# Performance work log

Hardware: AMD Instinct MI355X
Metric: run time of the kernel (lower is better)

Reference implementation:

```python
import jax, jax.numpy as jnp
import numpy as np

N_NODES = 100000
N_EDGES = 3200000

def setup_inputs() -> dict:
    key = jax.random.key(0)
    ks = jax.random.split(key, 16)
    x = jax.random.normal(ks[0], (N_NODES, 3), dtype=jnp.float32)
    edge_index = jax.random.randint(ks[1], (2, N_EDGES), 0, N_NODES, dtype=jnp.int32)
    def glorot(k, shape):
        fan = shape[0] + shape[-1]
        lim = jnp.sqrt(6.0 / fan)
        return jax.random.uniform(k, shape, jnp.float32, -lim, lim)
    params = {
        'W1': glorot(ks[2], (3, 32)),  'as1': glorot(ks[3], (2, 16)), 'ad1': glorot(ks[4], (2, 16)), 'b1': jnp.zeros((32,), jnp.float32),
        'W2': glorot(ks[5], (32, 32)), 'as2': glorot(ks[6], (2, 16)), 'ad2': glorot(ks[7], (2, 16)), 'b2': jnp.zeros((32,), jnp.float32),
        'W3': glorot(ks[8], (32, 8)),  'as3': glorot(ks[9], (1, 8)),  'ad3': glorot(ks[10], (1, 8)), 'b3': jnp.zeros((8,), jnp.float32),
        'Wo': glorot(ks[11], (8, 1)),  'bo': jnp.zeros((1,), jnp.float32),
    }
    return dict(x=x, edge_index=edge_index, **params)

def _gat_layer(x, src, dst, W, a_src, a_dst, bias, n_heads, c_out):
    # PyG GATConv: linear -> per-head attention logits -> leaky_relu -> segment softmax over dst -> scatter-weighted sum -> concat heads + bias
    N = x.shape[0]
    h = (x @ W).reshape(N, n_heads, c_out)              # [N,H,C]
    al_s = jnp.sum(h * a_src[None], axis=-1)            # [N,H]
    al_d = jnp.sum(h * a_dst[None], axis=-1)            # [N,H]
    logits = jax.nn.leaky_relu(al_s[src] + al_d[dst], 0.2)  # [E,H]
    m = jax.ops.segment_max(logits, dst, num_segments=N)
    e = jnp.exp(logits - m[dst])
    s = jax.ops.segment_sum(e, dst, num_segments=N)
    alpha = e / (s[dst] + 1e-16)                        # [E,H]
    msg = h[src] * alpha[:, :, None]                    # [E,H,C]
    out = jax.ops.segment_sum(msg, dst, num_segments=N) # [N,H,C]
    return out.reshape(N, n_heads * c_out) + bias

def reference(x, edge_index, W1, as1, ad1, b1, W2, as2, ad2, b2, W3, as3, ad3, b3, Wo, bo):
    N = x.shape[0]
    # add self loops (PyG GATConv default add_self_loops=True)
    loop = jnp.arange(N, dtype=edge_index.dtype)
    src = jnp.concatenate([edge_index[0], loop])
    dst = jnp.concatenate([edge_index[1], loop])
    h = jax.nn.elu(_gat_layer(x, src, dst, W1, as1, ad1, b1, 2, 16))
    h = jax.nn.elu(_gat_layer(h, src, dst, W2, as2, ad2, b2, 2, 16))
    h = jax.nn.elu(_gat_layer(h, src, dst, W3, as3, ad3, b3, 1, 8))
    return h @ Wo + bo
```

## Files before the change

kernel.cpp:

```cpp
#include <hip/hip_runtime.h>
#include <hip/hip_bf16.h>
#include <math.h>

#define DEVINL __device__ __forceinline__

DEVINL float loadIn(const void* p, long i, int bf) {
    return bf ? __bfloat162float(((const __hip_bfloat16*)p)[i])
              : ((const float*)p)[i];
}

DEVINL float leaky(float v) { return fmaxf(v, 0.2f * v); }

DEVINL unsigned pack_bf16(float a, float b) {
    __hip_bfloat16 x = __float2bfloat16(a), y = __float2bfloat16(b);
    unsigned short ux = *reinterpret_cast<unsigned short*>(&x);
    unsigned short uy = *reinterpret_cast<unsigned short*>(&y);
    return (unsigned)ux | ((unsigned)uy << 16);
}
DEVINL float lo16(unsigned u) { return __uint_as_float(u << 16); }
DEVINL float hi16(unsigned u) { return __uint_as_float(u & 0xFFFF0000u); }

__global__ __launch_bounds__(1024) void prep(const unsigned* __restrict__ x,
                                             int* __restrict__ flag,
                                             int* __restrict__ bcnt) {
    __shared__ int sh[1024];
    int t = threadIdx.x;
    bcnt[t] = 0;
    int cnt = 0;
    for (int i = t; i < 2048; i += 1024) {
        unsigned ex = (x[i] >> 7) & 0xFFu;
        if (ex >= 110u && ex <= 140u) cnt++;
    }
    sh[t] = cnt;
    __syncthreads();
    for (int s = 512; s > 0; s >>= 1) {
        if (t < s) sh[t] += sh[t + s];
        __syncthreads();
    }
    if (t == 0) *flag = (sh[0] >= 1200) ? 1 : 0;
}

__global__ __launch_bounds__(256) void bhist(const int* __restrict__ dst, int E,
                                             int* __restrict__ bcnt) {
    __shared__ int lh[512];
    for (int i = threadIdx.x; i < 512; i += 256) lh[i] = 0;
    __syncthreads();
    int stride = gridDim.x * 256;
    for (int e = blockIdx.x * 256 + threadIdx.x; e < E; e += stride)
        atomicAdd(&lh[dst[e] >> 8], 1);
    __syncthreads();
    for (int i = threadIdx.x; i < 512; i += 256)
        if (lh[i]) atomicAdd(&bcnt[i], lh[i]);
}

__global__ __launch_bounds__(1024) void bscan(const int* __restrict__ bcnt,
                                              int* __restrict__ bstart,
                                              int* __restrict__ bcur) {
    __shared__ int sA[1024], sB[1024];
    int t = threadIdx.x;
    int c = bcnt[t];
    sA[t] = c;
    __syncthreads();
    int* a = sA; int* b = sB;
    for (int off = 1; off < 1024; off <<= 1) {
        int v = a[t] + ((t >= off) ? a[t - off] : 0);
        __syncthreads();
        b[t] = v;
        __syncthreads();
        int* tp = a; a = b; b = tp;
    }
    int excl = a[t] - c;
    bstart[t] = excl;
    bcur[t] = excl;
    if (t == 1023) bstart[1024] = a[t];
}

#define CS_CHUNK 16384
__global__ __launch_bounds__(512) void block_scatter(
    const int* __restrict__ srcIdx, const int* __restrict__ dstIdx, int E,
    int* __restrict__ bcur, int* __restrict__ buf) {
    __shared__ int lh[512];
    __shared__ int lcur[512];
    int t = threadIdx.x;
    int e0 = blockIdx.x * CS_CHUNK;
    int e1 = e0 + CS_CHUNK; if (e1 > E) e1 = E;

    if (t < 512) lh[t] = 0;
    __syncthreads();
    for (int e = e0 + t; e < e1; e += 512)
        atomicAdd(&lh[dstIdx[e] >> 8], 1);
    __syncthreads();
    if (t < 512) {
        int c = lh[t];
        lcur[t] = c ? atomicAdd(&bcur[t], c) : 0;
    }
    __syncthreads();
    for (int e = e0 + t; e < e1; e += 512) {
        int d = dstIdx[e];
        int s = srcIdx[e];
        int pos = atomicAdd(&lcur[d >> 8], 1);
        buf[pos] = ((d & 255) << 17) | s;
    }
}

#define FS_CAP 10240
__global__ __launch_bounds__(256) void fine_scatter(
    const int* __restrict__ bstart, int* buf, int* ss,
    int* __restrict__ rp, int* __restrict__ cnt, int N) {
    __shared__ int stage[FS_CAP];
    __shared__ int hcnt[256];
    __shared__ int hA[256], hB[256];
    __shared__ int lcur[256];
    int bkt = blockIdx.x;
    int t = threadIdx.x;
    int s0 = bstart[bkt];
    int m = bstart[bkt + 1] - s0;
    if (m > FS_CAP) m = FS_CAP;

    for (int i = t; i < m; i += 256) stage[i] = buf[s0 + i];
    hcnt[t] = 0;
    __syncthreads();
    for (int i = t; i < m; i += 256) atomicAdd(&hcnt[stage[i] >> 17], 1);
    __syncthreads();
    hA[t] = hcnt[t];
    __syncthreads();
    int* a = hA; int* b = hB;
    for (int off = 1; off < 256; off <<= 1) {
        int v = a[t] + ((t >= off) ? a[t - off] : 0);
        __syncthreads();
        b[t] = v;
        __syncthreads();
        int* tp = a; a = b; b = tp;
    }
    {
        int excl = a[t] - hcnt[t];
        lcur[t] = s0 + excl;
        int node = bkt * 256 + t;
        if (node < N) {
            rp[node] = s0 + excl;
            cnt[node] = hcnt[t];
        }
    }
    __syncthreads();
    for (int i = t; i < m; i += 256) {
        int v = stage[i];
        int pos = atomicAdd(&lcur[v >> 17], 1);
        ss[pos] = v & 0x1FFFF;
    }
}

__global__ __launch_bounds__(256) void xprep(
    const void* __restrict__ x, const int* __restrict__ flagp,
    const void* __restrict__ W1, const void* __restrict__ as1,
    const void* __restrict__ ad1,
    float4* __restrict__ xp, float* __restrict__ cvec, int N)
{
    const int bf = *flagp;
    int n = blockIdx.x * 256 + threadIdx.x;
    if (n < N) {
        float4 v;
        v.x = loadIn(x, (long)n * 3 + 0, bf);
        v.y = loadIn(x, (long)n * 3 + 1, bf);
        v.z = loadIn(x, (long)n * 3 + 2, bf);
        v.w = 0.0f;
        xp[n] = v;
    }
    if (blockIdx.x == 0 && threadIdx.x < 12) {
        int t = threadIdx.x;
        int isd = t >= 6;
        int h = (t - 6 * isd) / 3;
        int k = (t - 6 * isd) % 3;
        const void* av = isd ? ad1 : as1;
        float s = 0.0f;
        for (int c = 0; c < 16; c++)
            s += loadIn(W1, k * 32 + h * 16 + c, bf) * loadIn(av, h * 16 + c, bf);
        cvec[t] = s;
    }
}

__global__ __launch_bounds__(256) void aggregate_l1(
    const int* __restrict__ rp_start, const int* __restrict__ cnt,
    const int* __restrict__ ss, const float4* __restrict__ xp,
    const float* __restrict__ cvec,
    const void* __restrict__ W1, const void* __restrict__ b1,
    const int* __restrict__ flagp,
    unsigned* __restrict__ xout, int N)
{
    const int bf = *flagp;
    __shared__ float Wl[96];
    __shared__ float bl[32];
    for (int i = threadIdx.x; i < 96; i += 256) Wl[i] = loadIn(W1, i, bf);
    for (int i = threadIdx.x; i < 32; i += 256) bl[i] = loadIn(b1, i, bf);
    __syncthreads();

    int lane = threadIdx.x & 63;
    int g = lane >> 4;
    int q = lane & 15;
    int wid = threadIdx.x >> 6;

    float cs[2][3], cd[2][3];
#pragma unroll
    for (int h = 0; h < 2; h++)
#pragma unroll
        for (int k = 0; k < 3; k++) {
            cs[h][k] = cvec[h * 3 + k];
            cd[h][k] = cvec[6 + h * 3 + k];
        }

    const int nstride = gridDim.x * 16;
    for (int node = blockIdx.x * 16 + wid * 4 + g; ; node += nstride) {
        if (node - g >= N) break;
        bool valid = node < N;
        int idx = valid ? node : 0;
        int start = rp_start[idx];
        int deg = valid ? cnt[idx] : 0;
        float4 xn = xp[idx];

        float alsn[2], aldn[2];
#pragma unroll
        for (int h = 0; h < 2; h++) {
            alsn[h] = xn.x * cs[h][0] + xn.y * cs[h][1] + xn.z * cs[h][2];
            aldn[h] = xn.x * cd[h][0] + xn.y * cd[h][1] + xn.z * cd[h][2];
        }

        float a00 = 0.f, a01 = 0.f, a02 = 0.f, s0 = 0.f;
        float a10 = 0.f, a11 = 0.f, a12 = 0.f, s1 = 0.f;

        if (q == 0 && valid) {
            float e0 = __expf(fminf(leaky(alsn[0] + aldn[0]), 80.0f));
            float e1 = __expf(fminf(leaky(alsn[1] + aldn[1]), 80.0f));
            a00 = e0 * xn.x; a01 = e0 * xn.y; a02 = e0 * xn.z; s0 = e0;
            a10 = e1 * xn.x; a11 = e1 * xn.y; a12 = e1 * xn.z; s1 = e1;
        }

        for (int kb = q; kb < deg; kb += 32) {
            int k2 = kb + 16;
            bool ok2 = k2 < deg;
            int sA = ss[start + kb];
            int sB = ss[start + (ok2 ? k2 : kb)];
            float4 xa = xp[sA];
            float4 xb = xp[sB];
            {
                float l0 = xa.x * cs[0][0] + xa.y * cs[0][1] + xa.z * cs[0][2] + aldn[0];
                float l1 = xa.x * cs[1][0] + xa.y * cs[1][1] + xa.z * cs[1][2] + aldn[1];
                float e0 = __expf(fminf(leaky(l0), 80.0f));
                float e1 = __expf(fminf(leaky(l1), 80.0f));
                a00 = fmaf(xa.x, e0, a00); a01 = fmaf(xa.y, e0, a01);
                a02 = fmaf(xa.z, e0, a02); s0 += e0;
                a10 = fmaf(xa.x, e1, a10); a11 = fmaf(xa.y, e1, a11);
                a12 = fmaf(xa.z, e1, a12); s1 += e1;
            }
            {
                float l0 = xb.x * cs[0][0] + xb.y * cs[0][1] + xb.z * cs[0][2] + aldn[0];
                float l1 = xb.x * cs[1][0] + xb.y * cs[1][1] + xb.z * cs[1][2] + aldn[1];
                float e0 = ok2 ? __expf(fminf(leaky(l0), 80.0f)) : 0.0f;
                float e1 = ok2 ? __expf(fminf(leaky(l1), 80.0f)) : 0.0f;
                a00 = fmaf(xb.x, e0, a00); a01 = fmaf(xb.y, e0, a01);
                a02 = fmaf(xb.z, e0, a02); s0 += e0;
                a10 = fmaf(xb.x, e1, a10); a11 = fmaf(xb.y, e1, a11);
                a12 = fmaf(xb.z, e1, a12); s1 += e1;
            }
        }

#pragma unroll
        for (int off = 1; off < 16; off <<= 1) {
            a00 += __shfl_xor(a00, off, 64); a01 += __shfl_xor(a01, off, 64);
            a02 += __shfl_xor(a02, off, 64); s0  += __shfl_xor(s0,  off, 64);
            a10 += __shfl_xor(a10, off, 64); a11 += __shfl_xor(a11, off, 64);
            a12 += __shfl_xor(a12, off, 64); s1  += __shfl_xor(s1,  off, 64);
        }

        if (valid) {
            int h = q >> 3;
            float inv = 1.0f / ((h ? s1 : s0) + 1e-16f);
            float g0 = (h ? a10 : a00) * inv;
            float g1 = (h ? a11 : a01) * inv;
            float g2 = (h ? a12 : a02) * inv;
            int c0 = 2 * q;
            float v0 = g0 * Wl[c0]      + g1 * Wl[32 + c0]      + g2 * Wl[64 + c0]      + bl[c0];
            float v1 = g0 * Wl[c0 + 1]  + g1 * Wl[32 + c0 + 1]  + g2 * Wl[64 + c0 + 1]  + bl[c0 + 1];
            v0 = v0 > 0.0f ? v0 : __expf(fminf(v0, 0.0f)) - 1.0f;
            v1 = v1 > 0.0f ? v1 : __expf(fminf(v1, 0.0f)) - 1.0f;
            xout[(long)node * 16 + q] = pack_bf16(v0, v1);
        }
    }
}

template <int XMODE, int C_IN, int H, int C>
__global__ __launch_bounds__(256) void node_transform(
    const void* __restrict__ xin, const int* __restrict__ flagp,
    const void* __restrict__ W, const void* __restrict__ a_s,
    const void* __restrict__ a_d,
    unsigned* __restrict__ h2, float* __restrict__ als,
    float* __restrict__ ald, int N)
{
    const int bf = *flagp;
    constexpr int HC = H * C;
    __shared__ float Ws[C_IN * HC];
    __shared__ float asS[HC];
    __shared__ float adS[HC];
    for (int i = threadIdx.x; i < C_IN * HC; i += 256) Ws[i] = loadIn(W, i, bf);
    for (int i = threadIdx.x; i < HC; i += 256) {
        asS[i] = loadIn(a_s, i, bf);
        adS[i] = loadIn(a_d, i, bf);
    }
    __syncthreads();

    int n = blockIdx.x * 256 + threadIdx.x;
    if (n >= N) return;

    float xv[C_IN];
    if (XMODE) {
        const uint4* x4 = (const uint4*)xin;
#pragma unroll
        for (int q = 0; q < C_IN / 8; q++) {
            uint4 w = x4[(long)n * (C_IN / 8) + q];
            xv[q * 8 + 0] = lo16(w.x); xv[q * 8 + 1] = hi16(w.x);
            xv[q * 8 + 2] = lo16(w.y); xv[q * 8 + 3] = hi16(w.y);
            xv[q * 8 + 4] = lo16(w.z); xv[q * 8 + 5] = hi16(w.z);
            xv[q * 8 + 6] = lo16(w.w); xv[q * 8 + 7] = hi16(w.w);
        }
    } else {
#pragma unroll
        for (int k = 0; k < C_IN; k++) xv[k] = loadIn(xin, (long)n * C_IN + k, bf);
    }

    float hv[HC];
#pragma unroll
    for (int j = 0; j < HC; j++) {
        float v = 0.0f;
#pragma unroll
        for (int k = 0; k < C_IN; k++) v = fmaf(xv[k], Ws[k * HC + j], v);
        hv[j] = v;
    }
#pragma unroll
    for (int jj = 0; jj < HC / 2; jj++)
        h2[(long)n * (HC / 2) + jj] = pack_bf16(hv[2 * jj], hv[2 * jj + 1]);

#pragma unroll
    for (int hh = 0; hh < H; hh++) {
        float vs = 0.0f, vd = 0.0f;
#pragma unroll
        for (int c = 0; c < C; c++) {
            vs = fmaf(hv[hh * C + c], asS[hh * C + c], vs);
            vd = fmaf(hv[hh * C + c], adS[hh * C + c], vd);
        }
        als[(long)n * H + hh] = vs;
        ald[(long)n * H + hh] = vd;
    }
}

template <int H, int C, int NCH, int UNR, int FUSE>
__global__ __launch_bounds__(256) void aggregate(
    const int* __restrict__ rp_start, const int* __restrict__ cnt,
    const int* __restrict__ ss,
    const unsigned* __restrict__ h2,
    const float* __restrict__ als, const float* __restrict__ ald,
    const void* __restrict__ bias, const void* __restrict__ Wo,
    const void* __restrict__ bo, const int* __restrict__ flagp,
    void* __restrict__ xout, int N)
{
    constexpr int HC = H * C;
    constexpr int J = HC / NCH;
    constexpr int EPW = 64 / J;
    constexpr int SLOTS = UNR * EPW;
    const int bf = *flagp;
    int lane = threadIdx.x & 63;
    int p = lane / J;
    int j = lane % J;
    int c0 = NCH * j;
    int head = c0 / C;
    const float* __restrict__ alsH = als + head;

    float bv[NCH];
#pragma unroll
    for (int i = 0; i < NCH; i++) bv[i] = loadIn(bias, c0 + i, bf);
    float wov[NCH];
    float bov = 0.0f;
    if constexpr (FUSE) {
#pragma unroll
        for (int i = 0; i < NCH; i++) wov[i] = loadIn(Wo, c0 + i, bf);
        bov = loadIn(bo, 0, bf);
    }

    const int nstride = gridDim.x << 2;
    const int node0 = (blockIdx.x << 2) + (threadIdx.x >> 6);
    if (node0 >= N) return;

    int nd0, nd1, st0, st1, dg0, dg1;
    float an0, an1, sa0, sa1;
    uint2 sq0, sq1; unsigned sw0, sw1;
    int sr0[UNR], sr1[UNR];
    float av0[UNR], av1[UNR];
    uint2 hq0[UNR], hq1[UNR];
    unsigned hw0[UNR], hw1[UNR];

#define AGG_LOADCSR(S, NODE) {                                              \
    int nn_ = (NODE); nd##S = nn_;                                          \
    int ii_ = nn_ < N ? nn_ : N - 1;                                        \
    st##S = rp_start[ii_];                                                  \
    dg##S = nn_ < N ? cnt[ii_] : 0;                                         \
    an##S = ald[ii_ * H + head];                                            \
    sa##S = alsH[ii_ * H];                                                  \
    if constexpr (NCH == 4) sq##S = ((const uint2*)h2)[ii_ * (HC / 4) + j]; \
    else sw##S = h2[ii_ * (HC / 2) + j]; }

#define AGG_ISSUE_SS(S) {                                                   \
    int dm1_ = dg##S > 0 ? dg##S - 1 : 0;                                   \
    _Pragma("unroll") for (int u = 0; u < UNR; u++) {                       \
        int k_ = p + u * EPW;                                               \
        sr##S[u] = ss[st##S + (k_ < dg##S ? k_ : dm1_)]; } }

#define AGG_ISSUE_G(S) {                                                    \
    _Pragma("unroll") for (int u = 0; u < UNR; u++) {                       \
        av##S[u] = alsH[sr##S[u] * H];                                      \
        if constexpr (NCH == 4)                                             \
            hq##S[u] = ((const uint2*)h2)[sr##S[u] * (HC / 4) + j];         \
        else hw##S[u] = h2[sr##S[u] * (HC / 2) + j]; } }

#define AGG_BODY(A, B) {                                                    \
    int node_c = nd##A, start_c = st##A, deg_c = dg##A;                     \
    float an_c = an##A, sa_c = sa##A;                                       \
    uint2 sq_c = sq##A; unsigned sw_c = sw##A; (void)sq_c; (void)sw_c;      \
                                             \
    AGG_ISSUE_G(B);                                                         \
              \
    AGG_LOADCSR(A, node_c + 2 * nstride);                                   \
                                                       \
    float acc[NCH]; float ssum = 0.0f;                                      \
    _Pragma("unroll") for (int i = 0; i < NCH; i++) acc[i] = 0.0f;          \
    if (p == 0) {                                                           \
        float es_ = __expf(fminf(leaky(sa_c + an_c), 80.0f));               \
        if constexpr (NCH == 4) {                                           \
            acc[0] = lo16(sq_c.x) * es_; acc[1] = hi16(sq_c.x) * es_;       \
            acc[2] = lo16(sq_c.y) * es_; acc[3] = hi16(sq_c.y) * es_;       \
        } else {                                                            \
            acc[0] = lo16(sw_c) * es_; acc[1] = hi16(sw_c) * es_;           \
        }                                                                   \
        ssum = es_;                                                         \
    }                                                                       \
    _Pragma("unroll") for (int u = 0; u < UNR; u++) {                       \
        int k_ = p + u * EPW;                                               \
        float e_ = (k_ < deg_c)                                             \
            ? __expf(fminf(leaky(av##A[u] + an_c), 80.0f)) : 0.0f;          \
        if constexpr (NCH == 4) {                                           \
            acc[0] = fmaf(lo16(hq##A[u].x), e_, acc[0]);                    \
            acc[1] = fmaf(hi16(hq##A[u].x), e_, acc[1]);                    \
            acc[2] = fmaf(lo16(hq##A[u].y), e_, acc[2]);                    \
            acc[3] = fmaf(hi16(hq##A[u].y), e_, acc[3]);                    \
        } else {                                                            \
            acc[0] = fmaf(lo16(hw##A[u]), e_, acc[0]);                      \
            acc[1] = fmaf(hi16(hw##A[u]), e_, acc[1]);                      \
        }                                                                   \
        ssum += e_;                                                         \
    }                                                                       \
                          \
    if (deg_c > SLOTS) {                                                    \
        for (int kb_ = SLOTS + p; kb_ < deg_c; kb_ += EPW) {                \
            int s_ = ss[start_c + kb_];                                     \
            float e_ = __expf(fminf(leaky(alsH[s_ * H] + an_c), 80.0f));    \
            if constexpr (NCH == 4) {                                       \
                uint2 hv_ = ((const uint2*)h2)[s_ * (HC / 4) + j];          \
                acc[0] = fmaf(lo16(hv_.x), e_, acc[0]);                     \
                acc[1] = fmaf(hi16(hv_.x), e_, acc[1]);                     \
                acc[2] = fmaf(lo16(hv_.y), e_, acc[2]);                     \
                acc[3] = fmaf(hi16(hv_.y), e_, acc[3]);                     \
            } else {                                                        \
                unsigned hv_ = h2[s_ * (HC / 2) + j];                       \
                acc[0] = fmaf(lo16(hv_), e_, acc[0]);                       \
                acc[1] = fmaf(hi16(hv_), e_, acc[1]);                       \
            }                                                               \
            ssum += e_;                                                     \
        }                                                                   \
    }                                                                       \
                \
    AGG_ISSUE_SS(A);                                                        \
                                                        \
    _Pragma("unroll") for (int off = J; off < 64; off <<= 1) {              \
        _Pragma("unroll") for (int i = 0; i < NCH; i++)                     \
            acc[i] += __shfl_xor(acc[i], off, 64);                          \
        ssum += __shfl_xor(ssum, off, 64);                                  \
    }                                                                       \
    float inv = 1.0f / (ssum + 1e-16f);                                     \
    float v[NCH];                                                           \
    _Pragma("unroll") for (int i = 0; i < NCH; i++) {                       \
        float t_ = acc[i] * inv + bv[i];                                    \
        v[i] = t_ > 0.0f ? t_ : __expf(fminf(t_, 0.0f)) - 1.0f;             \
    }                                                                       \
    if constexpr (FUSE) {                                                   \
        float r_ = 0.0f;                                                    \
        _Pragma("unroll") for (int i = 0; i < NCH; i++)                     \
            r_ = fmaf(v[i], wov[i], r_);                                    \
        _Pragma("unroll") for (int off = 1; off < J; off <<= 1)             \
            r_ += __shfl_xor(r_, off, 64);                                  \
        if (lane == 0 && node_c < N) {                                      \
            r_ += bov;                                                      \
            if (bf) ((__hip_bfloat16*)xout)[node_c] = __float2bfloat16(r_); \
            else    ((float*)xout)[node_c] = r_;                            \
        }                                                                   \
    } else {                                                                \
        if (p == 0 && node_c < N) {                                         \
            if constexpr (NCH == 4) {                                       \
                uint2 o_; o_.x = pack_bf16(v[0], v[1]);                     \
                o_.y = pack_bf16(v[2], v[3]);                               \
                ((uint2*)xout)[node_c * (HC / 4) + j] = o_;                 \
            } else {                                                        \
                ((unsigned*)xout)[node_c * (HC / 2) + j] =                  \
                    pack_bf16(v[0], v[1]);                                  \
            }                                                               \
        }                                                                   \
    } }

    AGG_LOADCSR(0, node0);
    AGG_LOADCSR(1, node0 + nstride);
    AGG_ISSUE_SS(0);
    AGG_ISSUE_G(0);
    AGG_ISSUE_SS(1);

    for (;;) {
        AGG_BODY(0, 1);
        if (nd1 >= N) break;
        AGG_BODY(1, 0);
        if (nd0 >= N) break;
    }

#undef AGG_LOADCSR
#undef AGG_ISSUE_SS
#undef AGG_ISSUE_G
#undef AGG_BODY
}

extern "C" void kernel_launch(void* const* d_in, const int* in_sizes, int n_in,
                              void* d_out, int out_size, void* d_ws, size_t ws_size,
                              hipStream_t stream) {
    const void* x   = d_in[0];
    const int*  ei  = (const int*)d_in[1];
    const void* W1  = d_in[2];
    const void* as1 = d_in[3];
    const void* ad1 = d_in[4];
    const void* b1  = d_in[5];
    const void* W2  = d_in[6];
    const void* as2 = d_in[7];
    const void* ad2 = d_in[8];
    const void* b2  = d_in[9];
    const void* W3  = d_in[10];
    const void* as3 = d_in[11];
    const void* ad3 = d_in[12];
    const void* b3  = d_in[13];
    const void* Wo  = d_in[14];
    const void* bo  = d_in[15];

    const int N = in_sizes[0] / 3;
    const int E = in_sizes[1] / 2;
    const int* ei0 = ei;
    const int* ei1 = ei + E;

    int* flag   = (int*)d_ws;
    int* bcnt   = flag + 64;
    int* bstart = bcnt + 1024;
    int* bcur   = bstart + 1088;
    int* cnt    = bcur + 1024;
    int* rp     = cnt + N;
    int* ss     = rp + N;
    float* als  = (float*)(ss + E);
    float* ald  = als + (long)N * 2;
    unsigned* A = (unsigned*)(ald + (long)N * 2);
    unsigned* h = A + (long)N * 16;
    float4* xp  = (float4*)(h + (long)N * 16);
    float* cvec = (float*)(xp + (long)N);

    const int B = 256;
    auto cdiv = [](long a, long b) { return (int)((a + b - 1) / b); };
    const int NBKT = cdiv(N, 256);

    const int aggBlocks = 2048;

    prep<<<1, 1024, 0, stream>>>((const unsigned*)x, flag, bcnt);
    xprep<<<cdiv(N, B), B, 0, stream>>>(x, flag, W1, as1, ad1, xp, cvec, N);
    bhist<<<256, B, 0, stream>>>(ei1, E, bcnt);
    bscan<<<1, 1024, 0, stream>>>(bcnt, bstart, bcur);
    block_scatter<<<cdiv(E, CS_CHUNK), 512, 0, stream>>>(ei0, ei1, E, bcur, ss);
    fine_scatter<<<NBKT, B, 0, stream>>>(bstart, ss, ss, rp, cnt, N);

    aggregate_l1<<<aggBlocks, B, 0, stream>>>(
        rp, cnt, ss, xp, cvec, W1, b1, flag, A, N);

    node_transform<1, 32, 2, 16><<<cdiv(N, B), B, 0, stream>>>(
        A, flag, W2, as2, ad2, h, als, ald, N);
    aggregate<2, 16, 4, 6, 0><<<aggBlocks, B, 0, stream>>>(
        rp, cnt, ss, h, als, ald, b2, nullptr, nullptr, flag, A, N);

    node_transform<1, 32, 1, 8><<<cdiv(N, B), B, 0, stream>>>(
        A, flag, W3, as3, ad3, h, als, ald, N);
    aggregate<1, 8, 2, 3, 1><<<aggBlocks, B, 0, stream>>>(
        rp, cnt, ss, h, als, ald, b3, Wo, bo, flag, d_out, N);
}
```

Measured before the change: 314.2 us.

## Load edge source indices once per lane and broadcast via shuffles

Each lane now loads one source index and its attention logits (both heads as a float2). The exp of the edge logits is computed once per edge rather than redundantly by every channel-group lane, and the index and weight are then distributed to the consuming lanes with wave shuffles. This removes duplicate index and logit gathers and duplicate exp work across the J lanes handling the same edge. In exchange it adds several shuffles per unrolled slot and a select between heads.

Result: no change. 314.5 us (+0.1%).

```diff
diff --git a/kernel.cpp b/kernel.cpp
--- a/kernel.cpp
+++ b/kernel.cpp
@@ -370,7 +370,6 @@
     int j = lane % J;
     int c0 = NCH * j;
     int head = c0 / C;
-    const float* __restrict__ alsH = als + head;
 
     float bv[NCH];
 #pragma unroll
@@ -388,10 +387,10 @@
     if (node0 >= N) return;
 
     int nd0, nd1, st0, st1, dg0, dg1;
-    float an0, an1, sa0, sa1;
+    float2 an0, an1, sa0, sa1;
     uint2 sq0, sq1; unsigned sw0, sw1;
-    int sr0[UNR], sr1[UNR];
-    float av0[UNR], av1[UNR];
+    int sv0, sv1;
+    float2 af0, af1;
     uint2 hq0[UNR], hq1[UNR];
     unsigned hw0[UNR], hw1[UNR];
 
@@ -400,37 +399,46 @@
     int ii_ = nn_ < N ? nn_ : N - 1;                                        \
     st##S = rp_start[ii_];                                                  \
     dg##S = nn_ < N ? cnt[ii_] : 0;                                         \
-    an##S = ald[ii_ * H + head];                                            \
-    sa##S = alsH[ii_ * H];                                                  \
+    if constexpr (H == 2) {                                                 \
+        an##S = ((const float2*)ald)[ii_];                                  \
+        sa##S = ((const float2*)als)[ii_];                                  \
+    } else {                                                                \
+        an##S.x = ald[ii_]; an##S.y = 0.0f;                                 \
+        sa##S.x = als[ii_]; sa##S.y = 0.0f;                                 \
+    }                                                                       \
     if constexpr (NCH == 4) sq##S = ((const uint2*)h2)[ii_ * (HC / 4) + j]; \
     else sw##S = h2[ii_ * (HC / 2) + j]; }
 
 #define AGG_ISSUE_SS(S) {                                                   \
     int dm1_ = dg##S > 0 ? dg##S - 1 : 0;                                   \
+    int kk_ = (lane < dg##S && lane < SLOTS) ? lane : dm1_;                 \
+    sv##S = ss[st##S + kk_]; }
+
+#define AGG_ISSUE_G(S) {                                                    \
+    if constexpr (H == 2) af##S = ((const float2*)als)[sv##S];              \
+    else { af##S.x = als[sv##S]; af##S.y = 0.0f; }                          \
     _Pragma("unroll") for (int u = 0; u < UNR; u++) {                       \
-        int k_ = p + u * EPW;                                               \
-        sr##S[u] = ss[st##S + (k_ < dg##S ? k_ : dm1_)]; } }
-
-#define AGG_ISSUE_G(S) {                                                    \
-    _Pragma("unroll") for (int u = 0; u < UNR; u++) {                       \
-        av##S[u] = alsH[sr##S[u] * H];                                      \
+        int sru_ = __shfl(sv##S, p + u * EPW, 64);                          \
         if constexpr (NCH == 4)                                             \
-            hq##S[u] = ((const uint2*)h2)[sr##S[u] * (HC / 4) + j];         \
-        else hw##S[u] = h2[sr##S[u] * (HC / 2) + j]; } }
+            hq##S[u] = ((const uint2*)h2)[sru_ * (HC / 4) + j];             \
+        else hw##S[u] = h2[sru_ * (HC / 2) + j]; } }
 
 #define AGG_BODY(A, B) {                                                    \
     int node_c = nd##A, start_c = st##A, deg_c = dg##A;                     \
-    float an_c = an##A, sa_c = sa##A;                                       \
+    float2 an_c = an##A, sa_c = sa##A;                                      \
+    float2 af_c = af##A;                                                    \
     uint2 sq_c = sq##A; unsigned sw_c = sw##A; (void)sq_c; (void)sw_c;      \
                                              \
     AGG_ISSUE_G(B);                                                         \
               \
     AGG_LOADCSR(A, node_c + 2 * nstride);                                   \
                                                        \
+    float an_h = (H == 2) ? (head ? an_c.y : an_c.x) : an_c.x;              \
+    float sa_h = (H == 2) ? (head ? sa_c.y : sa_c.x) : sa_c.x;              \
     float acc[NCH]; float ssum = 0.0f;                                      \
     _Pragma("unroll") for (int i = 0; i < NCH; i++) acc[i] = 0.0f;          \
     if (p == 0) {                                                           \
-        float es_ = __expf(fminf(leaky(sa_c + an_c), 80.0f));               \
+        float es_ = __expf(fminf(leaky(sa_h + an_h), 80.0f));               \
         if constexpr (NCH == 4) {                                           \
             acc[0] = lo16(sq_c.x) * es_; acc[1] = hi16(sq_c.x) * es_;       \
             acc[2] = lo16(sq_c.y) * es_; acc[3] = hi16(sq_c.y) * es_;       \
@@ -439,10 +447,24 @@
         }                                                                   \
         ssum = es_;                                                         \
     }                                                                       \
+              \
+    bool okl_ = (lane < SLOTS) && (lane < deg_c);                           \
+    float e0v_ = okl_                                                       \
+        ? __expf(fminf(leaky(af_c.x + an_c.x), 80.0f)) : 0.0f;              \
+    float e1v_ = 0.0f;                                                      \
+    if constexpr (H == 2)                                                   \
+        e1v_ = okl_                                                         \
+            ? __expf(fminf(leaky(af_c.y + an_c.y), 80.0f)) : 0.0f;          \
+               \
     _Pragma("unroll") for (int u = 0; u < UNR; u++) {                       \
-        int k_ = p + u * EPW;                                               \
-        float e_ = (k_ < deg_c)                                             \
-            ? __expf(fminf(leaky(av##A[u] + an_c), 80.0f)) : 0.0f;          \
+        float e_;                                                           \
+        if constexpr (H == 2) {                                             \
+            float s0_ = __shfl(e0v_, p + u * EPW, 64);                      \
+            float s1_ = __shfl(e1v_, p + u * EPW, 64);                      \
+            e_ = head ? s1_ : s0_;                                          \
+        } else {                                                            \
+            e_ = __shfl(e0v_, p + u * EPW, 64);                             \
+        }                                                                   \
         if constexpr (NCH == 4) {                                           \
             acc[0] = fmaf(lo16(hq##A[u].x), e_, acc[0]);                    \
             acc[1] = fmaf(hi16(hq##A[u].x), e_, acc[1]);                    \
@@ -454,11 +476,12 @@
         }                                                                   \
         ssum += e_;                                                         \
     }                                                                       \
-                          \
+            \
     if (deg_c > SLOTS) {                                                    \
         for (int kb_ = SLOTS + p; kb_ < deg_c; kb_ += EPW) {                \
             int s_ = ss[start_c + kb_];                                     \
-            float e_ = __expf(fminf(leaky(alsH[s_ * H] + an_c), 80.0f));    \
+            float a_ = als[s_ * H + head];                                  \
+            float e_ = __expf(fminf(leaky(a_ + an_h), 80.0f));              \
             if constexpr (NCH == 4) {                                       \
                 uint2 hv_ = ((const uint2*)h2)[s_ * (HC / 4) + j];          \
                 acc[0] = fmaf(lo16(hv_.x), e_, acc[0]);                     \
@@ -473,7 +496,7 @@
             ssum += e_;                                                     \
         }                                                                   \
     }                                                                       \
-                \
+        \
     AGG_ISSUE_SS(A);                                                        \
                                                         \
     _Pragma("unroll") for (int off = J; off < 64; off <<= 1) {              \
```
